# Performance work log

Hardware: AMD Instinct MI355X
Metric: run time of the kernel (lower is better)

## Reference

```python
import jax, jax.numpy as jnp
from jax import lax
import numpy as np

MAX_SEQ_LEN = 8192
B, S, D = 8, 8192, 1024
LN_EPS = 1e-5

# ---------- static lattice structure (pure Python, replicates original incl. quirks) ----------

def _gen_spine(max_len):
    s = [0, 2, 4]
    while True:
        nxt = 2 * s[-1] + 2 * s[-2] + 2 * s[-3]
        if nxt >= max_len:
            break
        s.append(nxt)
    return s

def _imm_anc(spine, pos):
    if pos in spine:
        i = spine.index(pos)
        if i >= 3:
            return [spine[i - 1], spine[i - 2], spine[i - 3]]
    return []

def _analyze(spine, pos):
    # BFS over ancestors; NOTE: levels[level+1] is OVERWRITTEN per popped node,
    # exactly as in the original torch code.
    visited = {pos}
    levels = {0: [pos]}
    queue = [(pos, 0)]
    while queue:
        cur, lvl = queue.pop(0)
        if lvl >= 9:
            break
        newl = []
        for a in _imm_anc(spine, cur):
            if a not in visited and a >= 0:
                visited.add(a)
                newl.append(a)
                queue.append((a, lvl + 1))
        if newl:
            levels[lvl + 1] = list(newl)
    max_depth = max(levels.keys())
    pc = {pos: 1}
    for lvl in sorted(levels.keys(), reverse=True):
        for node in levels[lvl]:
            if node == pos:
                continue
            if lvl == max_depth:
                pc[node] = 1
                continue
            c = 0
            for ch in levels.get(lvl + 1, []):
                if node in _imm_anc(spine, ch):
                    c += pc.get(ch, 0)
            if lvl != 0:
                pc[node] = c
    pc.pop(pos, None)
    return levels, pc

def _structures(seq_len):
    spine = _gen_spine(MAX_SEQ_LEN)
    out = []
    for pos in spine:
        if pos >= seq_len or pos < 3:
            continue
        levels, pc = _analyze(spine, pos)
        anc, cnt = [], []
        for lvl in levels:  # dict insertion order == level order, as in torch
            if lvl > 0:
                for a in levels[lvl]:
                    if a < seq_len:
                        anc.append(a)
                        cnt.append(float(pc.get(a, 1)))
        if anc:
            out.append((pos, np.array(anc, np.int32), np.array(cnt, np.float32)))
    return out

# ---------- neural pieces ----------

def _gru_last(seq, w_ih, w_hh, b_ih, b_hh):
    # seq: [B, K, D]; single-layer batch_first GRU, h0 = 0; returns last hidden [B, D]
    d = w_hh.shape[1]
    def step(h, xt):
        gi = xt @ w_ih.T + b_ih   # [B, 3D]
        gh = h @ w_hh.T + b_hh
        i_r, i_z, i_n = jnp.split(gi, 3, axis=-1)
        h_r, h_z, h_n = jnp.split(gh, 3, axis=-1)
        r = jax.nn.sigmoid(i_r + h_r)
        z = jax.nn.sigmoid(i_z + h_z)
        n = jnp.tanh(i_n + r * h_n)
        return (1.0 - z) * n + z * h, None
    h0 = jnp.zeros((seq.shape[0], d), seq.dtype)
    hT, _ = lax.scan(step, h0, jnp.swapaxes(seq, 0, 1))
    return hT

def reference(x, pw_w1, pw_b1, pw_w2, pw_b2, msg_w, msg_b, ln_g, ln_b,
              gru_w_ih, gru_w_hh, gru_b_ih, gru_b_hh, gate_w, gate_b):
    structs = _structures(x.shape[1])
    out = x
    for pos, anc, cnt in structs:
        # path weights: Linear(1,64)->ReLU->Linear(64,1)->Softplus  on counts [K,1]
        c = jnp.asarray(cnt)[:, None]
        w = jax.nn.softplus(jnp.squeeze(jax.nn.relu(c @ pw_w1.T + pw_b1) @ pw_w2.T + pw_b2))  # [K]
        h_anc = x[:, anc, :]                         # [B, K, D] gather
        h_cur = x[:, pos, :]                         # [B, D]
        pair = jnp.concatenate([h_anc, jnp.broadcast_to(h_cur[:, None, :], h_anc.shape)], axis=-1)
        m = pair @ msg_w.T + msg_b                   # [B, K, D]
        mu = m.mean(-1, keepdims=True)
        var = ((m - mu) ** 2).mean(-1, keepdims=True)
        m = (m - mu) / jnp.sqrt(var + LN_EPS) * ln_g + ln_b
        m = jax.nn.gelu(m, approximate=False)
        m = m * w[None, :, None]                     # path-weighted messages
        agg = _gru_last(m, gru_w_ih, gru_w_hh, gru_b_ih, gru_b_hh)  # [B, D]
        g = jax.nn.sigmoid(jnp.concatenate([agg, h_cur], axis=-1) @ gate_w.T + gate_b)
        out = out.at[:, pos, :].set(g * agg + (1.0 - g) * h_cur)
    return out

def setup_inputs() -> dict:
    key = jax.random.key(0)
    ks = jax.random.split(key, 8)
    def n(k, shape, s=0.02):
        return jax.random.normal(k, shape, jnp.float32) * s
    return {
        "x": jax.random.normal(ks[0], (B, S, D), jnp.float32),
        "pw_w1": n(ks[1], (64, 1), 0.5), "pw_b1": jnp.zeros((64,), jnp.float32),
        "pw_w2": n(ks[2], (1, 64), 0.5), "pw_b2": jnp.zeros((1,), jnp.float32),
        "msg_w": n(ks[3], (D, 2 * D)), "msg_b": jnp.zeros((D,), jnp.float32),
        "ln_g": jnp.ones((D,), jnp.float32), "ln_b": jnp.zeros((D,), jnp.float32),
        "gru_w_ih": n(ks[4], (3 * D, D)), "gru_w_hh": n(ks[5], (3 * D, D)),
        "gru_b_ih": jnp.zeros((3 * D,), jnp.float32), "gru_b_hh": jnp.zeros((3 * D,), jnp.float32),
        "gate_w": n(ks[6], (D, 2 * D)), "gate_b": jnp.zeros((D,), jnp.float32),
    }
```

## Files before the change

### kernel.cpp

```cpp
#include <hip/hip_runtime.h>
#include <math.h>
#include <string.h>

#define SEQ 8192
#define DIM 1024
#define NBATCH 8

typedef float vf4 __attribute__((ext_vector_type(4)));

struct SDesc {
  int n, Tmax, totalRows;
  int pos[8], A[8], rowbase[8];
  int anc[8][8];
  float cnt[8][8];
  int nu;
  int upos[16];
  int up_of_s[8];
  int s_of_rr[32], a_of_rr[32], ua_of_rr[32];
};

static SDesc build_structs() {
  SDesc H{};
  int spine[24];
  int ns = 3; spine[0] = 0; spine[1] = 2; spine[2] = 4;
  for (;;) {
    long nxt = 2L * (spine[ns-1] + spine[ns-2] + spine[ns-3]);
    if (nxt >= SEQ) break;
    spine[ns++] = (int)nxt;
  }
  int rb = 0;
  for (int i = 0; i < ns; ++i) {
    int pos = spine[i];
    if (pos < 3) continue;
    bool visited[24] = {false};
    int levels[12][8]; int lcnt[12];
    for (int l = 0; l < 12; ++l) lcnt[l] = 0;
    levels[0][0] = i; lcnt[0] = 1; visited[i] = true;
    int qidx[64], qlvl[64], qh = 0, qt = 0;
    qidx[qt] = i; qlvl[qt] = 0; qt++;
    int maxd = 0;
    while (qh < qt) {
      int cur = qidx[qh], lvl = qlvl[qh]; qh++;
      if (lvl >= 9) break;
      int newl[8], nn = 0;
      if (cur >= 3) {
        for (int d = 1; d <= 3; ++d) {
          int a = cur - d;
          if (!visited[a]) { visited[a] = true; newl[nn++] = a; qidx[qt] = a; qlvl[qt] = lvl + 1; qt++; }
        }
      }
      if (nn) {
        lcnt[lvl+1] = nn;
        for (int k = 0; k < nn; ++k) levels[lvl+1][k] = newl[k];
        if (lvl + 1 > maxd) maxd = lvl + 1;
      }
    }
    float pcv[24]; bool pcs[24];
    for (int k = 0; k < 24; ++k) { pcv[k] = 0.f; pcs[k] = false; }
    pcv[i] = 1.f; pcs[i] = true;
    for (int lvl = maxd; lvl >= 0; --lvl) {
      for (int nidx = 0; nidx < lcnt[lvl]; ++nidx) {
        int node = levels[lvl][nidx];
        if (node == i) continue;
        if (lvl == maxd) { pcv[node] = 1.f; pcs[node] = true; continue; }
        float c = 0.f;
        for (int cidx = 0; cidx < lcnt[lvl+1]; ++cidx) {
          int ch = levels[lvl+1][cidx];
          if (ch >= 3 && node >= ch - 3 && node <= ch - 1) c += pcs[ch] ? pcv[ch] : 0.f;
        }
        if (lvl != 0) { pcv[node] = c; pcs[node] = true; }
      }
    }
    int A = 0;
    int sidx = H.n;
    for (int lvl = 1; lvl <= maxd; ++lvl) {
      for (int nidx = 0; nidx < lcnt[lvl]; ++nidx) {
        int node = levels[lvl][nidx];
        H.anc[sidx][A] = spine[node];
        H.cnt[sidx][A] = pcs[node] ? pcv[node] : 1.f;
        A++;
      }
    }
    if (A == 0) continue;
    H.pos[sidx] = pos; H.A[sidx] = A; H.rowbase[sidx] = rb; rb += A;
    H.n++;
  }
  H.totalRows = rb;
  H.Tmax = 0;
  for (int s = 0; s < H.n; ++s) if (H.A[s] > H.Tmax) H.Tmax = H.A[s];
  int vals[128], nv = 0;
  for (int s = 0; s < H.n; ++s) {
    vals[nv++] = H.pos[s];
    for (int a = 0; a < H.A[s]; ++a) vals[nv++] = H.anc[s][a];
  }
  H.nu = 0;
  for (int i = 0; i < nv; ++i) {
    bool seen = false;
    for (int u = 0; u < H.nu; ++u) if (H.upos[u] == vals[i]) { seen = true; break; }
    if (!seen) H.upos[H.nu++] = vals[i];
  }
  for (int i = 0; i < H.nu; ++i)
    for (int j2 = i + 1; j2 < H.nu; ++j2)
      if (H.upos[j2] < H.upos[i]) { int t = H.upos[i]; H.upos[i] = H.upos[j2]; H.upos[j2] = t; }
  auto uidx = [&](int v) { for (int u = 0; u < H.nu; ++u) if (H.upos[u] == v) return u; return 0; };
  for (int s = 0; s < H.n; ++s) {
    H.up_of_s[s] = uidx(H.pos[s]);
    for (int a = 0; a < H.A[s]; ++a) {
      int rr = H.rowbase[s] + a;
      H.s_of_rr[rr] = s; H.a_of_rr[rr] = a; H.ua_of_rr[rr] = uidx(H.anc[s][a]);
    }
  }
  return H;
}


__device__ __forceinline__ void do_copy(const vf4* __restrict__ src, vf4* __restrict__ dst,
                                        int q, int nc, int start4, int n4) {
  for (int i = q * 256 + threadIdx.x; i < n4; i += nc * 256) {
    vf4 v = __builtin_nontemporal_load(&src[start4 + i]);
    __builtin_nontemporal_store(v, &dst[start4 + i]);
  }
}

__device__ __forceinline__ float wred(float v) {
  #pragma unroll
  for (int off = 32; off; off >>= 1) v += __shfl_xor(v, off);
  return v;
}

__device__ __forceinline__ float dot4(vf4 a, vf4 b) {
  return a.x * b.x + a.y * b.y + a.z * b.z + a.w * b.w;
}


__global__ __launch_bounds__(256, 4) void k_T(SDesc sd, const float* __restrict__ x,
    const float* __restrict__ msg_w, float* __restrict__ T,
    const float* __restrict__ w1, const float* __restrict__ b1,
    const float* __restrict__ w2, const float* __restrict__ b2, float* __restrict__ wout,
    int NC, const vf4* __restrict__ csrc, vf4* __restrict__ cdst, int cstart, int cn) {
  int p = blockIdx.x;
  const int NMAIN = 1280;
  if (p == NMAIN) {
    int t = threadIdx.x;
    int s = t >> 3, a = t & 7;
    if (t < 64 && s < sd.n && a < sd.A[s]) {
      float v = sd.cnt[s][a];
      float acc = 0.f;
      for (int i = 0; i < 64; ++i) {
        float h = v * w1[i] + b1[i];
        if (h > 0.f) acc += h * w2[i];
      }
      float o = acc + b2[0];
      float sp = (o > 0.f) ? (o + log1pf(expf(-o))) : log1pf(expf(o));
      wout[s * 8 + a] = sp;
    }
    return;
  }
  if (p > NMAIN) { do_copy(csrc, cdst, p - NMAIN - 1, NC, cstart, cn); return; }
  int q = p % 128, rt = p / 128;
  int jt = (q & 7) * 16 + (q >> 3);

  int wave = threadIdx.x >> 6, lane = threadIdx.x & 63;
  int jc0 = jt * 16 + wave * 4;
  const vf4* mw4 = (const vf4*)msg_w;
  size_t b0 = (size_t)((jc0 + 0) & 1023) * 512 + (((jc0 + 0) >> 10) << 8);
  size_t b1_ = (size_t)((jc0 + 1) & 1023) * 512 + (((jc0 + 1) >> 10) << 8);
  size_t b2_ = (size_t)((jc0 + 2) & 1023) * 512 + (((jc0 + 2) >> 10) << 8);
  size_t b3 = (size_t)((jc0 + 3) & 1023) * 512 + (((jc0 + 3) >> 10) << 8);
  vf4 w0[4], w1v[4], w2v[4], w3[4];
  #pragma unroll
  for (int c = 0; c < 4; ++c) {
    w0[c]  = mw4[b0  + c * 64 + lane];
    w1v[c] = mw4[b1_ + c * 64 + lane];
    w2v[c] = mw4[b2_ + c * 64 + lane];
    w3[c]  = mw4[b3  + c * 64 + lane];
  }
  const vf4* x4 = (const vf4*)x;
  #pragma unroll 2
  for (int r = 0; r < 8; ++r) {
    int row = rt * 8 + r; int u = row >> 3, b = row & 7;
    size_t rb4 = ((size_t)b * SEQ + sd.upos[u]) * 256;
    vf4 a0 = x4[rb4 + 0 * 64 + lane], a1 = x4[rb4 + 1 * 64 + lane];
    vf4 a2 = x4[rb4 + 2 * 64 + lane], a3 = x4[rb4 + 3 * 64 + lane];
    float s0 = dot4(w0[0],  a0) + dot4(w0[1],  a1) + dot4(w0[2],  a2) + dot4(w0[3],  a3);
    float s1 = dot4(w1v[0], a0) + dot4(w1v[1], a1) + dot4(w1v[2], a2) + dot4(w1v[3], a3);
    float s2 = dot4(w2v[0], a0) + dot4(w2v[1], a1) + dot4(w2v[2], a2) + dot4(w2v[3], a3);
    float s3 = dot4(w3[0],  a0) + dot4(w3[1],  a1) + dot4(w3[2],  a2) + dot4(w3[3],  a3);
    s0 = wred(s0); s1 = wred(s1); s2 = wred(s2); s3 = wred(s3);
    if (lane == 0) {
      float* tp = T + (size_t)row * 2048 + jc0;
      tp[0] = s0; tp[1] = s1; tp[2] = s2; tp[3] = s3;
    }
  }
}

__global__ __launch_bounds__(256) void k_ln(SDesc sd, const float* __restrict__ ln_g,
    const float* __restrict__ ln_b, const float* __restrict__ msg_b,
    const float* __restrict__ wsc, const float* __restrict__ T, float* __restrict__ mseq,
    int M, int NC, const vf4* __restrict__ csrc, vf4* __restrict__ cdst, int cstart, int cn) {
  int p = blockIdx.x;
  if (p >= M) { do_copy(csrc, cdst, p - M, NC, cstart, cn); return; }
  int rr = p >> 3, b = p & 7;
  int s = sd.s_of_rr[rr], a = sd.a_of_rr[rr];
  int ua = sd.ua_of_rr[rr], up = sd.up_of_s[s];
  float wmul = wsc[s * 8 + a];
  const vf4* Tl = (const vf4*)(T + ((size_t)ua * 8 + b) * 2048);
  const vf4* Tr = (const vf4*)(T + ((size_t)up * 8 + b) * 2048 + 1024);
  const vf4* mb = (const vf4*)msg_b;
  int t = threadIdx.x;
  vf4 vl = Tl[t], vr = Tr[t], vb = mb[t];
  vf4 v; v.x = vl.x + vr.x + vb.x; v.y = vl.y + vr.y + vb.y;
  v.z = vl.z + vr.z + vb.z; v.w = vl.w + vr.w + vb.w;
  float sum = v.x + v.y + v.z + v.w;
  float sq  = v.x * v.x + v.y * v.y + v.z * v.z + v.w * v.w;
  #pragma unroll
  for (int off = 32; off; off >>= 1) { sum += __shfl_xor(sum, off); sq += __shfl_xor(sq, off); }
  __shared__ float s1[4], s2[4];
  int wave = t >> 6, lane = t & 63;
  if (lane == 0) { s1[wave] = sum; s2[wave] = sq; }
  __syncthreads();
  sum = s1[0] + s1[1] + s1[2] + s1[3];
  sq  = s2[0] + s2[1] + s2[2] + s2[3];
  float mu  = sum * (1.f / 1024.f);
  float var = sq * (1.f / 1024.f) - mu * mu;
  float inv = rsqrtf(var + 1e-5f);
  vf4 g4 = ((const vf4*)ln_g)[t];
  vf4 b4 = ((const vf4*)ln_b)[t];
  float o[4]  = {v.x, v.y, v.z, v.w};
  float gg[4] = {g4.x, g4.y, g4.z, g4.w};
  float bb[4] = {b4.x, b4.y, b4.z, b4.w};
  #pragma unroll
  for (int i = 0; i < 4; ++i) {
    float u = (o[i] - mu) * inv * gg[i] + bb[i];
    float ge = 0.5f * u * (1.f + erff(u * 0.70710678118654752f));
    o[i] = ge * wmul;
  }
  vf4 ov; ov.x = o[0]; ov.y = o[1]; ov.z = o[2]; ov.w = o[3];
  ((vf4*)(mseq + (size_t)p * DIM))[t] = ov;
}

__global__ __launch_bounds__(256, 4) void k_gi(const float* __restrict__ mseq,
    const float* __restrict__ wih, const float* __restrict__ bih, float* __restrict__ gi,
    int NC, const vf4* __restrict__ csrc, vf4* __restrict__ cdst, int cstart, int cn) {
  int p = blockIdx.x;
  const int NMAIN = 2880;
  if (p >= NMAIN) { do_copy(csrc, cdst, p - NMAIN, NC, cstart, cn); return; }
  int q = p % 192, rt = p / 192;
  int jt = (q & 7) * 24 + (q >> 3);

  int wave = threadIdx.x >> 6, lane = threadIdx.x & 63;
  int j0 = jt * 16 + wave * 4;
  const vf4* wp4 = (const vf4*)wih;
  vf4 w0[4], w1[4], w2[4], w3[4];
  #pragma unroll
  for (int c = 0; c < 4; ++c) {
    w0[c] = wp4[(size_t)(j0 + 0) * 256 + c * 64 + lane];
    w1[c] = wp4[(size_t)(j0 + 1) * 256 + c * 64 + lane];
    w2[c] = wp4[(size_t)(j0 + 2) * 256 + c * 64 + lane];
    w3[c] = wp4[(size_t)(j0 + 3) * 256 + c * 64 + lane];
  }
  const vf4* m4 = (const vf4*)mseq;
  #pragma unroll 2
  for (int r = 0; r < 16; ++r) {
    int row = rt * 16 + r;
    size_t rb4 = (size_t)row * 256;
    vf4 a0 = m4[rb4 + 0 * 64 + lane], a1 = m4[rb4 + 1 * 64 + lane];
    vf4 a2 = m4[rb4 + 2 * 64 + lane], a3 = m4[rb4 + 3 * 64 + lane];
    float s0 = dot4(w0[0], a0) + dot4(w0[1], a1) + dot4(w0[2], a2) + dot4(w0[3], a3);
    float s1 = dot4(w1[0], a0) + dot4(w1[1], a1) + dot4(w1[2], a2) + dot4(w1[3], a3);
    float s2 = dot4(w2[0], a0) + dot4(w2[1], a1) + dot4(w2[2], a2) + dot4(w2[3], a3);
    float s3 = dot4(w3[0], a0) + dot4(w3[1], a1) + dot4(w3[2], a2) + dot4(w3[3], a3);
    s0 = wred(s0); s1 = wred(s1); s2 = wred(s2); s3 = wred(s3);
    if (lane == 0) {
      float* gp = gi + (size_t)row * 3072 + j0;
      gp[0] = s0 + bih[j0 + 0]; gp[1] = s1 + bih[j0 + 1];
      gp[2] = s2 + bih[j0 + 2]; gp[3] = s3 + bih[j0 + 3];
    }
  }
}

__global__ __launch_bounds__(256, 4) void k_step(SDesc sd, int t,
    const float* __restrict__ whh, const float* __restrict__ bhh,
    const float* __restrict__ gi, const float* __restrict__ hold, float* __restrict__ hnew,
    int NC, const vf4* __restrict__ csrc, vf4* __restrict__ cdst, int cstart, int cn) {
  int p = blockIdx.x;
  const int NMAIN = 7 * 256;
  if (p >= NMAIN) { do_copy(csrc, cdst, p - NMAIN, NC, cstart, cn); return; }
  int q = p & 255, s = p >> 8;
  int jt = (q & 7) * 32 + (q >> 3);
  int t0 = sd.Tmax - sd.A[s];
  if (t < t0) return;
  int a = t - t0;

  int wave = threadIdx.x >> 6, lane = threadIdx.x & 63;
  int j = jt * 4 + wave;
  int girow0 = (sd.rowbase[s] + a) * 8;

  if (a == 0) {
    if (lane < 8) {
      int r = lane;
      const float* gp = gi + (size_t)(girow0 + r) * 3072;
      float rg = 1.f / (1.f + expf(-(gp[j] + bhh[j])));
      float zg = 1.f / (1.f + expf(-(gp[1024 + j] + bhh[1024 + j])));
      float ng = tanhf(gp[2048 + j] + rg * bhh[2048 + j]);
      hnew[(size_t)(s * 8 + r) * DIM + j] = (1.f - zg) * ng;
    }
    return;
  }

  const vf4* wp4 = (const vf4*)whh;
  vf4 wr[4], wz[4], wn[4];
  #pragma unroll
  for (int c = 0; c < 4; ++c) {
    wr[c] = wp4[(size_t)j * 256 + c * 64 + lane];
    wz[c] = wp4[(size_t)(1024 + j) * 256 + c * 64 + lane];
    wn[c] = wp4[(size_t)(2048 + j) * 256 + c * 64 + lane];
  }
  float bj_r = bhh[j], bj_z = bhh[1024 + j], bj_n = bhh[2048 + j];
  const vf4* h4 = (const vf4*)hold;
  #pragma unroll 2
  for (int r = 0; r < 8; ++r) {
    int srow = s * 8 + r;
    size_t rb4 = (size_t)srow * 256;
    const float* gp = gi + (size_t)(girow0 + r) * 3072;
    float gir = gp[j], giz = gp[1024 + j], gin = gp[2048 + j];
    vf4 a0 = h4[rb4 + 0 * 64 + lane], a1 = h4[rb4 + 1 * 64 + lane];
    vf4 a2 = h4[rb4 + 2 * 64 + lane], a3 = h4[rb4 + 3 * 64 + lane];
    float ar = dot4(wr[0], a0) + dot4(wr[1], a1) + dot4(wr[2], a2) + dot4(wr[3], a3);
    float az = dot4(wz[0], a0) + dot4(wz[1], a1) + dot4(wz[2], a2) + dot4(wz[3], a3);
    float an = dot4(wn[0], a0) + dot4(wn[1], a1) + dot4(wn[2], a2) + dot4(wn[3], a3);
    ar = wred(ar); az = wred(az); an = wred(an);
    if (lane == 0) {
      float rg = 1.f / (1.f + expf(-(gir + ar + bj_r)));
      float zg = 1.f / (1.f + expf(-(giz + az + bj_z)));
      float ng = tanhf(gin + rg * (an + bj_n));
      float ho = hold[(size_t)srow * DIM + j];
      hnew[(size_t)srow * DIM + j] = (1.f - zg) * ng + zg * ho;
    }
  }
}

__global__ __launch_bounds__(256, 4) void k_gate(SDesc sd, const float* __restrict__ x,
    const float* __restrict__ gw, const float* __restrict__ gb,
    const float* __restrict__ hfin, float* __restrict__ out) {
  int p = blockIdx.x;
  int q = p % 128, rt = p / 128;
  int jt = (q & 7) * 16 + (q >> 3);

  int wave = threadIdx.x >> 6, lane = threadIdx.x & 63;
  int j0 = jt * 8 + wave * 2;
  const vf4* g4p = (const vf4*)gw;
  vf4 wL0[4], wR0[4], wL1[4], wR1[4];
  #pragma unroll
  for (int c = 0; c < 4; ++c) {
    wL0[c] = g4p[(size_t)(j0 + 0) * 512 + c * 64 + lane];
    wR0[c] = g4p[(size_t)(j0 + 0) * 512 + 256 + c * 64 + lane];
    wL1[c] = g4p[(size_t)(j0 + 1) * 512 + c * 64 + lane];
    wR1[c] = g4p[(size_t)(j0 + 1) * 512 + 256 + c * 64 + lane];
  }
  const vf4* h4 = (const vf4*)hfin;
  const vf4* x4 = (const vf4*)x;
  #pragma unroll 2
  for (int r = 0; r < 8; ++r) {
    int row = rt * 8 + r; int s = row >> 3, b = row & 7;
    size_t ab4 = (size_t)row * 256;
    size_t xb4 = ((size_t)b * SEQ + sd.pos[s]) * 256;
    vf4 a0 = h4[ab4 + 0 * 64 + lane], a1 = h4[ab4 + 1 * 64 + lane];
    vf4 a2 = h4[ab4 + 2 * 64 + lane], a3 = h4[ab4 + 3 * 64 + lane];
    vf4 x0 = x4[xb4 + 0 * 64 + lane], x1 = x4[xb4 + 1 * 64 + lane];
    vf4 x2 = x4[xb4 + 2 * 64 + lane], x3 = x4[xb4 + 3 * 64 + lane];
    float s0 = dot4(wL0[0], a0) + dot4(wL0[1], a1) + dot4(wL0[2], a2) + dot4(wL0[3], a3)
             + dot4(wR0[0], x0) + dot4(wR0[1], x1) + dot4(wR0[2], x2) + dot4(wR0[3], x3);
    float s1 = dot4(wL1[0], a0) + dot4(wL1[1], a1) + dot4(wL1[2], a2) + dot4(wL1[3], a3)
             + dot4(wR1[0], x0) + dot4(wR1[1], x1) + dot4(wR1[2], x2) + dot4(wR1[3], x3);
    s0 = wred(s0); s1 = wred(s1);
    if (lane == 0) {
      #pragma unroll
      for (int jj = 0; jj < 2; ++jj) {
        int j = j0 + jj;
        float sv = jj ? s1 : s0;
        float g = 1.f / (1.f + expf(-(sv + gb[j])));
        float agg = hfin[(size_t)row * DIM + j];
        float hc  = x[((size_t)b * SEQ + sd.pos[s]) * DIM + j];
        out[((size_t)b * SEQ + sd.pos[s]) * DIM + j] = g * agg + (1.f - g) * hc;
      }
    }
  }
}


extern "C" void kernel_launch(void* const* d_in, const int* in_sizes, int n_in,
                              void* d_out, int out_size, void* d_ws, size_t ws_size,
                              hipStream_t stream) {
  const float* x      = (const float*)d_in[0];
  const float* pw_w1  = (const float*)d_in[1];
  const float* pw_b1  = (const float*)d_in[2];
  const float* pw_w2  = (const float*)d_in[3];
  const float* pw_b2  = (const float*)d_in[4];
  const float* msg_w  = (const float*)d_in[5];
  const float* msg_b  = (const float*)d_in[6];
  const float* ln_g   = (const float*)d_in[7];
  const float* ln_b   = (const float*)d_in[8];
  const float* w_ih   = (const float*)d_in[9];
  const float* w_hh   = (const float*)d_in[10];
  const float* b_ih   = (const float*)d_in[11];
  const float* b_hh   = (const float*)d_in[12];
  const float* gate_w = (const float*)d_in[13];
  const float* gate_b = (const float*)d_in[14];
  float* out = (float*)d_out;
  float* ws  = (float*)d_ws;

  SDesc sd = build_structs();
  const int M = sd.totalRows * 8;

  float* wout = ws;
  float* T    = wout + 64;
  float* mseq = T + (size_t)sd.nu * 8 * 2048;
  float* gi   = mseq + (size_t)240 * DIM;
  float* h0   = gi + (size_t)240 * 3072;
  float* h1   = h0 + (size_t)sd.n * 8 * DIM;

  const vf4* x4 = (const vf4*)x;
  vf4* out4 = (vf4*)out;
  const int TOTAL4 = (NBATCH * SEQ * DIM) / 4;

  const int c_T  = 2200000;
  const int c_ln = 2400000;
  const int c_gi = 1800000;
  const int c_s0 = 2600000;
  const int c_s  = 1900000;

  int off = 0;
  k_T<<<1280 + 1 + 1024, 256, 0, stream>>>(sd, x, msg_w, T,
                                           pw_w1, pw_b1, pw_w2, pw_b2, wout,
                                           1024, x4, out4, off, c_T);
  off += c_T;

  k_ln<<<M + 1280, 256, 0, stream>>>(sd, ln_g, ln_b, msg_b, wout, T, mseq,
                                     M, 1280, x4, out4, off, c_ln);
  off += c_ln;

  k_gi<<<2880 + 1024, 256, 0, stream>>>(mseq, w_ih, b_ih, gi, 1024, x4, out4, off, c_gi);
  off += c_gi;

  for (int t = 0; t < sd.Tmax; ++t) {
    const float* hr = (t & 1) ? h1 : h0;
    float*       hw = (t & 1) ? h0 : h1;
    int cnt = (t == 0) ? c_s0 : (t == sd.Tmax - 1) ? (TOTAL4 - off) : c_s;
    k_step<<<7 * 256 + 1280, 256, 0, stream>>>(sd, t, w_hh, b_hh, gi, hr, hw,
                                               1280, x4, out4, off, cnt);
    off += cnt;
  }
  const float* hfin = (sd.Tmax & 1) ? h1 : h0;

  k_gate<<<128 * 7, 256, 0, stream>>>(sd, x, gate_w, gate_b, hfin, out);

  (void)in_sizes; (void)n_in; (void)out_size; (void)ws_size;
}
```

Baseline: 266.1 us.

## Fold background copy into all blocks, hoist GRU step 0, shrink grids

Drops the dedicated copy-only blocks. Every block of each phase kernel now runs its compute work and then takes a grid-strided share of the x→out copy. The first GRU step (zero hidden state) moves into the input-projection kernel, so the step loop runs from t=1 to 4 with Tmax hardcoded. The step and gate kernels now loop over all structures inside one block instead of spreading them over blocks, which cuts the grid size and reloads fewer weights. The price is less parallelism in the recurrent steps and hardcoded structure constants (Tmax, 240 rows, 56 rows). The k_gi launch also covers only 1920 of the 240×3072 outputs per row tile, with 24 rows per block, and its correctness depends on that arithmetic.

```diff
diff --git a/kernel.cpp b/kernel.cpp
--- a/kernel.cpp
+++ b/kernel.cpp
@@ -1,6 +1,5 @@
 #include <hip/hip_runtime.h>
 #include <math.h>
-#include <string.h>
 
 #define SEQ 8192
 #define DIM 1024
@@ -114,14 +113,6 @@
 }
 
 
-__device__ __forceinline__ void do_copy(const vf4* __restrict__ src, vf4* __restrict__ dst,
-                                        int q, int nc, int start4, int n4) {
-  for (int i = q * 256 + threadIdx.x; i < n4; i += nc * 256) {
-    vf4 v = __builtin_nontemporal_load(&src[start4 + i]);
-    __builtin_nontemporal_store(v, &dst[start4 + i]);
-  }
-}
-
 __device__ __forceinline__ float wred(float v) {
   #pragma unroll
   for (int off = 32; off; off >>= 1) v += __shfl_xor(v, off);
@@ -132,12 +123,21 @@
   return a.x * b.x + a.y * b.y + a.z * b.z + a.w * b.w;
 }
 
+__device__ __forceinline__ void phase_copy(const vf4* __restrict__ src,
+                                           vf4* __restrict__ dst, int start, int cnt) {
+  int stride = gridDim.x * 256;
+  for (int i = blockIdx.x * 256 + threadIdx.x; i < cnt; i += stride) {
+    vf4 v = __builtin_nontemporal_load(&src[start + i]);
+    __builtin_nontemporal_store(v, &dst[start + i]);
+  }
+}
+
 
 __global__ __launch_bounds__(256, 4) void k_T(SDesc sd, const float* __restrict__ x,
     const float* __restrict__ msg_w, float* __restrict__ T,
     const float* __restrict__ w1, const float* __restrict__ b1,
     const float* __restrict__ w2, const float* __restrict__ b2, float* __restrict__ wout,
-    int NC, const vf4* __restrict__ csrc, vf4* __restrict__ cdst, int cstart, int cn) {
+    const vf4* __restrict__ csrc, vf4* __restrict__ cdst, int cstart, int cn) {
   int p = blockIdx.x;
   const int NMAIN = 1280;
   if (p == NMAIN) {
@@ -151,163 +151,167 @@
         if (h > 0.f) acc += h * w2[i];
       }
       float o = acc + b2[0];
-      float sp = (o > 0.f) ? (o + log1pf(expf(-o))) : log1pf(expf(o));
-      wout[s * 8 + a] = sp;
-    }
-    return;
-  }
-  if (p > NMAIN) { do_copy(csrc, cdst, p - NMAIN - 1, NC, cstart, cn); return; }
-  int q = p % 128, rt = p / 128;
-  int jt = (q & 7) * 16 + (q >> 3);
-
-  int wave = threadIdx.x >> 6, lane = threadIdx.x & 63;
-  int jc0 = jt * 16 + wave * 4;
-  const vf4* mw4 = (const vf4*)msg_w;
-  size_t b0 = (size_t)((jc0 + 0) & 1023) * 512 + (((jc0 + 0) >> 10) << 8);
-  size_t b1_ = (size_t)((jc0 + 1) & 1023) * 512 + (((jc0 + 1) >> 10) << 8);
-  size_t b2_ = (size_t)((jc0 + 2) & 1023) * 512 + (((jc0 + 2) >> 10) << 8);
-  size_t b3 = (size_t)((jc0 + 3) & 1023) * 512 + (((jc0 + 3) >> 10) << 8);
-  vf4 w0[4], w1v[4], w2v[4], w3[4];
-  #pragma unroll
-  for (int c = 0; c < 4; ++c) {
-    w0[c]  = mw4[b0  + c * 64 + lane];
-    w1v[c] = mw4[b1_ + c * 64 + lane];
-    w2v[c] = mw4[b2_ + c * 64 + lane];
-    w3[c]  = mw4[b3  + c * 64 + lane];
-  }
-  const vf4* x4 = (const vf4*)x;
-  #pragma unroll 2
-  for (int r = 0; r < 8; ++r) {
-    int row = rt * 8 + r; int u = row >> 3, b = row & 7;
-    size_t rb4 = ((size_t)b * SEQ + sd.upos[u]) * 256;
-    vf4 a0 = x4[rb4 + 0 * 64 + lane], a1 = x4[rb4 + 1 * 64 + lane];
-    vf4 a2 = x4[rb4 + 2 * 64 + lane], a3 = x4[rb4 + 3 * 64 + lane];
-    float s0 = dot4(w0[0],  a0) + dot4(w0[1],  a1) + dot4(w0[2],  a2) + dot4(w0[3],  a3);
-    float s1 = dot4(w1v[0], a0) + dot4(w1v[1], a1) + dot4(w1v[2], a2) + dot4(w1v[3], a3);
-    float s2 = dot4(w2v[0], a0) + dot4(w2v[1], a1) + dot4(w2v[2], a2) + dot4(w2v[3], a3);
-    float s3 = dot4(w3[0],  a0) + dot4(w3[1],  a1) + dot4(w3[2],  a2) + dot4(w3[3],  a3);
-    s0 = wred(s0); s1 = wred(s1); s2 = wred(s2); s3 = wred(s3);
-    if (lane == 0) {
-      float* tp = T + (size_t)row * 2048 + jc0;
-      tp[0] = s0; tp[1] = s1; tp[2] = s2; tp[3] = s3;
-    }
-  }
+      wout[s * 8 + a] = (o > 0.f) ? (o + log1pf(expf(-o))) : log1pf(expf(o));
+    }
+  } else {
+    int q = p % 128, rt = p / 128;
+    int jt = (q & 7) * 16 + (q >> 3);
+    int wave = threadIdx.x >> 6, lane = threadIdx.x & 63;
+    int jc0 = jt * 16 + wave * 4;
+    const vf4* mw4 = (const vf4*)msg_w;
+    size_t wb0 = (size_t)((jc0 + 0) & 1023) * 512 + ((size_t)((jc0 + 0) >> 10) << 8);
+    size_t wb1 = (size_t)((jc0 + 1) & 1023) * 512 + ((size_t)((jc0 + 1) >> 10) << 8);
+    size_t wb2 = (size_t)((jc0 + 2) & 1023) * 512 + ((size_t)((jc0 + 2) >> 10) << 8);
+    size_t wb3 = (size_t)((jc0 + 3) & 1023) * 512 + ((size_t)((jc0 + 3) >> 10) << 8);
+    vf4 tw0[4], tw1[4], tw2[4], tw3[4];
+    #pragma unroll
+    for (int c = 0; c < 4; ++c) {
+      tw0[c] = mw4[wb0 + c * 64 + lane];
+      tw1[c] = mw4[wb1 + c * 64 + lane];
+      tw2[c] = mw4[wb2 + c * 64 + lane];
+      tw3[c] = mw4[wb3 + c * 64 + lane];
+    }
+    const vf4* x4 = (const vf4*)x;
+    #pragma unroll 2
+    for (int r = 0; r < 8; ++r) {
+      int row = rt * 8 + r; int uq = row >> 3, bb = row & 7;
+      size_t rb4 = ((size_t)bb * SEQ + sd.upos[uq]) * 256;
+      vf4 a0 = x4[rb4 + 0 * 64 + lane], a1 = x4[rb4 + 1 * 64 + lane];
+      vf4 a2 = x4[rb4 + 2 * 64 + lane], a3 = x4[rb4 + 3 * 64 + lane];
+      float s0 = dot4(tw0[0], a0) + dot4(tw0[1], a1) + dot4(tw0[2], a2) + dot4(tw0[3], a3);
+      float s1 = dot4(tw1[0], a0) + dot4(tw1[1], a1) + dot4(tw1[2], a2) + dot4(tw1[3], a3);
+      float s2 = dot4(tw2[0], a0) + dot4(tw2[1], a1) + dot4(tw2[2], a2) + dot4(tw2[3], a3);
+      float s3 = dot4(tw3[0], a0) + dot4(tw3[1], a1) + dot4(tw3[2], a2) + dot4(tw3[3], a3);
+      s0 = wred(s0); s1 = wred(s1); s2 = wred(s2); s3 = wred(s3);
+      if (lane == 0) {
+        float* tp = T + (size_t)row * 2048 + jc0;
+        tp[0] = s0; tp[1] = s1; tp[2] = s2; tp[3] = s3;
+      }
+    }
+  }
+  phase_copy(csrc, cdst, cstart, cn);
 }
 
 __global__ __launch_bounds__(256) void k_ln(SDesc sd, const float* __restrict__ ln_g,
     const float* __restrict__ ln_b, const float* __restrict__ msg_b,
     const float* __restrict__ wsc, const float* __restrict__ T, float* __restrict__ mseq,
-    int M, int NC, const vf4* __restrict__ csrc, vf4* __restrict__ cdst, int cstart, int cn) {
+    const vf4* __restrict__ csrc, vf4* __restrict__ cdst, int cstart, int cn) {
   int p = blockIdx.x;
-  if (p >= M) { do_copy(csrc, cdst, p - M, NC, cstart, cn); return; }
-  int rr = p >> 3, b = p & 7;
-  int s = sd.s_of_rr[rr], a = sd.a_of_rr[rr];
-  int ua = sd.ua_of_rr[rr], up = sd.up_of_s[s];
-  float wmul = wsc[s * 8 + a];
-  const vf4* Tl = (const vf4*)(T + ((size_t)ua * 8 + b) * 2048);
-  const vf4* Tr = (const vf4*)(T + ((size_t)up * 8 + b) * 2048 + 1024);
-  const vf4* mb = (const vf4*)msg_b;
-  int t = threadIdx.x;
-  vf4 vl = Tl[t], vr = Tr[t], vb = mb[t];
-  vf4 v; v.x = vl.x + vr.x + vb.x; v.y = vl.y + vr.y + vb.y;
-  v.z = vl.z + vr.z + vb.z; v.w = vl.w + vr.w + vb.w;
-  float sum = v.x + v.y + v.z + v.w;
-  float sq  = v.x * v.x + v.y * v.y + v.z * v.z + v.w * v.w;
-  #pragma unroll
-  for (int off = 32; off; off >>= 1) { sum += __shfl_xor(sum, off); sq += __shfl_xor(sq, off); }
-  __shared__ float s1[4], s2[4];
-  int wave = t >> 6, lane = t & 63;
-  if (lane == 0) { s1[wave] = sum; s2[wave] = sq; }
-  __syncthreads();
-  sum = s1[0] + s1[1] + s1[2] + s1[3];
-  sq  = s2[0] + s2[1] + s2[2] + s2[3];
-  float mu  = sum * (1.f / 1024.f);
-  float var = sq * (1.f / 1024.f) - mu * mu;
-  float inv = rsqrtf(var + 1e-5f);
-  vf4 g4 = ((const vf4*)ln_g)[t];
-  vf4 b4 = ((const vf4*)ln_b)[t];
-  float o[4]  = {v.x, v.y, v.z, v.w};
-  float gg[4] = {g4.x, g4.y, g4.z, g4.w};
-  float bb[4] = {b4.x, b4.y, b4.z, b4.w};
-  #pragma unroll
-  for (int i = 0; i < 4; ++i) {
-    float u = (o[i] - mu) * inv * gg[i] + bb[i];
-    float ge = 0.5f * u * (1.f + erff(u * 0.70710678118654752f));
-    o[i] = ge * wmul;
-  }
-  vf4 ov; ov.x = o[0]; ov.y = o[1]; ov.z = o[2]; ov.w = o[3];
-  ((vf4*)(mseq + (size_t)p * DIM))[t] = ov;
-}
-
-__global__ __launch_bounds__(256, 4) void k_gi(const float* __restrict__ mseq,
-    const float* __restrict__ wih, const float* __restrict__ bih, float* __restrict__ gi,
-    int NC, const vf4* __restrict__ csrc, vf4* __restrict__ cdst, int cstart, int cn) {
+  if (p < 240) {
+    int rr = p >> 3, bb = p & 7;
+    int s = sd.s_of_rr[rr], aa = sd.a_of_rr[rr];
+    int ua = sd.ua_of_rr[rr], up = sd.up_of_s[s];
+    float wmul = wsc[s * 8 + aa];
+    const vf4* Tl = (const vf4*)(T + ((size_t)ua * 8 + bb) * 2048);
+    const vf4* Tr = (const vf4*)(T + ((size_t)up * 8 + bb) * 2048 + 1024);
+    const vf4* mb = (const vf4*)msg_b;
+    int t = threadIdx.x;
+    vf4 vl = Tl[t], vr = Tr[t], vb = mb[t];
+    vf4 v; v.x = vl.x + vr.x + vb.x; v.y = vl.y + vr.y + vb.y;
+    v.z = vl.z + vr.z + vb.z; v.w = vl.w + vr.w + vb.w;
+    float sum = v.x + v.y + v.z + v.w;
+    float sq  = v.x * v.x + v.y * v.y + v.z * v.z + v.w * v.w;
+    #pragma unroll
+    for (int off = 32; off; off >>= 1) { sum += __shfl_xor(sum, off); sq += __shfl_xor(sq, off); }
+    __shared__ float s1[4], s2[4];
+    int wave = t >> 6, lane = t & 63;
+    if (lane == 0) { s1[wave] = sum; s2[wave] = sq; }
+    __syncthreads();
+    sum = s1[0] + s1[1] + s1[2] + s1[3];
+    sq  = s2[0] + s2[1] + s2[2] + s2[3];
+    float mu  = sum * (1.f / 1024.f);
+    float var = sq * (1.f / 1024.f) - mu * mu;
+    float inv = rsqrtf(var + 1e-5f);
+    vf4 g4 = ((const vf4*)ln_g)[t];
+    vf4 b4 = ((const vf4*)ln_b)[t];
+    float o[4]  = {v.x, v.y, v.z, v.w};
+    float gg[4] = {g4.x, g4.y, g4.z, g4.w};
+    float bb2[4] = {b4.x, b4.y, b4.z, b4.w};
+    #pragma unroll
+    for (int i = 0; i < 4; ++i) {
+      float u = (o[i] - mu) * inv * gg[i] + bb2[i];
+      float ge = 0.5f * u * (1.f + erff(u * 0.70710678118654752f));
+      o[i] = ge * wmul;
+    }
+    vf4 ov; ov.x = o[0]; ov.y = o[1]; ov.z = o[2]; ov.w = o[3];
+    ((vf4*)(mseq + (size_t)p * DIM))[t] = ov;
+  }
+  phase_copy(csrc, cdst, cstart, cn);
+}
+
+__global__ __launch_bounds__(256, 4) void k_gi(SDesc sd, const float* __restrict__ mseq,
+    const float* __restrict__ wih, const float* __restrict__ bih,
+    const float* __restrict__ bhh, float* __restrict__ gi, float* __restrict__ h1,
+    const vf4* __restrict__ csrc, vf4* __restrict__ cdst, int cstart, int cn) {
   int p = blockIdx.x;
-  const int NMAIN = 2880;
-  if (p >= NMAIN) { do_copy(csrc, cdst, p - NMAIN, NC, cstart, cn); return; }
-  int q = p % 192, rt = p / 192;
-  int jt = (q & 7) * 24 + (q >> 3);
-
-  int wave = threadIdx.x >> 6, lane = threadIdx.x & 63;
-  int j0 = jt * 16 + wave * 4;
-  const vf4* wp4 = (const vf4*)wih;
-  vf4 w0[4], w1[4], w2[4], w3[4];
-  #pragma unroll
-  for (int c = 0; c < 4; ++c) {
-    w0[c] = wp4[(size_t)(j0 + 0) * 256 + c * 64 + lane];
-    w1[c] = wp4[(size_t)(j0 + 1) * 256 + c * 64 + lane];
-    w2[c] = wp4[(size_t)(j0 + 2) * 256 + c * 64 + lane];
-    w3[c] = wp4[(size_t)(j0 + 3) * 256 + c * 64 + lane];
-  }
-  const vf4* m4 = (const vf4*)mseq;
-  #pragma unroll 2
-  for (int r = 0; r < 16; ++r) {
-    int row = rt * 16 + r;
-    size_t rb4 = (size_t)row * 256;
-    vf4 a0 = m4[rb4 + 0 * 64 + lane], a1 = m4[rb4 + 1 * 64 + lane];
-    vf4 a2 = m4[rb4 + 2 * 64 + lane], a3 = m4[rb4 + 3 * 64 + lane];
-    float s0 = dot4(w0[0], a0) + dot4(w0[1], a1) + dot4(w0[2], a2) + dot4(w0[3], a3);
-    float s1 = dot4(w1[0], a0) + dot4(w1[1], a1) + dot4(w1[2], a2) + dot4(w1[3], a3);
-    float s2 = dot4(w2[0], a0) + dot4(w2[1], a1) + dot4(w2[2], a2) + dot4(w2[3], a3);
-    float s3 = dot4(w3[0], a0) + dot4(w3[1], a1) + dot4(w3[2], a2) + dot4(w3[3], a3);
-    s0 = wred(s0); s1 = wred(s1); s2 = wred(s2); s3 = wred(s3);
-    if (lane == 0) {
-      float* gp = gi + (size_t)row * 3072 + j0;
-      gp[0] = s0 + bih[j0 + 0]; gp[1] = s1 + bih[j0 + 1];
-      gp[2] = s2 + bih[j0 + 2]; gp[3] = s3 + bih[j0 + 3];
-    }
-  }
+  {
+    int q = p % 192, rt = p / 192;
+    int jt = (q & 7) * 24 + (q >> 3);
+    int wave = threadIdx.x >> 6, lane = threadIdx.x & 63;
+    int j0 = jt * 16 + wave * 4;
+    const vf4* wp4 = (const vf4*)wih;
+    vf4 w0[4], w1[4], w2[4], w3[4];
+    #pragma unroll
+    for (int c = 0; c < 4; ++c) {
+      w0[c] = wp4[(size_t)(j0 + 0) * 256 + c * 64 + lane];
+      w1[c] = wp4[(size_t)(j0 + 1) * 256 + c * 64 + lane];
+      w2[c] = wp4[(size_t)(j0 + 2) * 256 + c * 64 + lane];
+      w3[c] = wp4[(size_t)(j0 + 3) * 256 + c * 64 + lane];
+    }
+    const vf4* m4 = (const vf4*)mseq;
+    for (int r = 0; r < 24; ++r) {
+      int row = rt * 24 + r;
+      size_t rb4 = (size_t)row * 256;
+      vf4 a0 = m4[rb4 + 0 * 64 + lane], a1 = m4[rb4 + 1 * 64 + lane];
+      vf4 a2 = m4[rb4 + 2 * 64 + lane], a3 = m4[rb4 + 3 * 64 + lane];
+      float s0 = dot4(w0[0], a0) + dot4(w0[1], a1) + dot4(w0[2], a2) + dot4(w0[3], a3);
+      float s1 = dot4(w1[0], a0) + dot4(w1[1], a1) + dot4(w1[2], a2) + dot4(w1[3], a3);
+      float s2 = dot4(w2[0], a0) + dot4(w2[1], a1) + dot4(w2[2], a2) + dot4(w2[3], a3);
+      float s3 = dot4(w3[0], a0) + dot4(w3[1], a1) + dot4(w3[2], a2) + dot4(w3[3], a3);
+      s0 = wred(s0); s1 = wred(s1); s2 = wred(s2); s3 = wred(s3);
+      if (lane == 0) {
+        float sv[4] = {s0, s1, s2, s3};
+        float* gp = gi + (size_t)row * 3072;
+        int rr = row >> 3;
+        int s = sd.s_of_rr[rr];
+        bool st0 = (sd.a_of_rr[rr] == 0 && sd.A[s] == sd.Tmax);
+        #pragma unroll
+        for (int jj = 0; jj < 4; ++jj) {
+          int jg = j0 + jj;
+          float val = sv[jj] + bih[jg];
+          gp[jg] = val;
+        }
+        if (st0) {
+        }
+      }
+    }
+  }
+  {
+    int tid = blockIdx.x * 256 + threadIdx.x;
+    int total = 240 * DIM;
+    for (int i = tid; i < total; i += gridDim.x * 256) {
+      int row = i >> 10, j = i & 1023;
+      int rr = row >> 3;
+      int s = sd.s_of_rr[rr];
+      if (sd.a_of_rr[rr] == 0 && sd.A[s] == sd.Tmax) {
+        const float* gp = gi + (size_t)row * 3072;
+        float rg = 1.f / (1.f + expf(-(gp[j] + bhh[j])));
+        float zg = 1.f / (1.f + expf(-(gp[1024 + j] + bhh[1024 + j])));
+        float ng = tanhf(gp[2048 + j] + rg * bhh[2048 + j]);
+        h1[(size_t)(s * 8 + (row & 7)) * DIM + j] = (1.f - zg) * ng;
+      }
+    }
+  }
+  phase_copy(csrc, cdst, cstart, cn);
 }
 
 __global__ __launch_bounds__(256, 4) void k_step(SDesc sd, int t,
     const float* __restrict__ whh, const float* __restrict__ bhh,
     const float* __restrict__ gi, const float* __restrict__ hold, float* __restrict__ hnew,
-    int NC, const vf4* __restrict__ csrc, vf4* __restrict__ cdst, int cstart, int cn) {
+    const vf4* __restrict__ csrc, vf4* __restrict__ cdst, int cstart, int cn) {
   int p = blockIdx.x;
-  const int NMAIN = 7 * 256;
-  if (p >= NMAIN) { do_copy(csrc, cdst, p - NMAIN, NC, cstart, cn); return; }
-  int q = p & 255, s = p >> 8;
-  int jt = (q & 7) * 32 + (q >> 3);
-  int t0 = sd.Tmax - sd.A[s];
-  if (t < t0) return;
-  int a = t - t0;
-
   int wave = threadIdx.x >> 6, lane = threadIdx.x & 63;
-  int j = jt * 4 + wave;
-  int girow0 = (sd.rowbase[s] + a) * 8;
-
-  if (a == 0) {
-    if (lane < 8) {
-      int r = lane;
-      const float* gp = gi + (size_t)(girow0 + r) * 3072;
-      float rg = 1.f / (1.f + expf(-(gp[j] + bhh[j])));
-      float zg = 1.f / (1.f + expf(-(gp[1024 + j] + bhh[1024 + j])));
-      float ng = tanhf(gp[2048 + j] + rg * bhh[2048 + j]);
-      hnew[(size_t)(s * 8 + r) * DIM + j] = (1.f - zg) * ng;
-    }
-    return;
-  }
-
+  int j = p * 4 + wave;
   const vf4* wp4 = (const vf4*)whh;
   vf4 wr[4], wz[4], wn[4];
   #pragma unroll
@@ -318,37 +322,53 @@
   }
   float bj_r = bhh[j], bj_z = bhh[1024 + j], bj_n = bhh[2048 + j];
   const vf4* h4 = (const vf4*)hold;
-  #pragma unroll 2
-  for (int r = 0; r < 8; ++r) {
-    int srow = s * 8 + r;
-    size_t rb4 = (size_t)srow * 256;
-    const float* gp = gi + (size_t)(girow0 + r) * 3072;
-    float gir = gp[j], giz = gp[1024 + j], gin = gp[2048 + j];
-    vf4 a0 = h4[rb4 + 0 * 64 + lane], a1 = h4[rb4 + 1 * 64 + lane];
-    vf4 a2 = h4[rb4 + 2 * 64 + lane], a3 = h4[rb4 + 3 * 64 + lane];
-    float ar = dot4(wr[0], a0) + dot4(wr[1], a1) + dot4(wr[2], a2) + dot4(wr[3], a3);
-    float az = dot4(wz[0], a0) + dot4(wz[1], a1) + dot4(wz[2], a2) + dot4(wz[3], a3);
-    float an = dot4(wn[0], a0) + dot4(wn[1], a1) + dot4(wn[2], a2) + dot4(wn[3], a3);
-    ar = wred(ar); az = wred(az); an = wred(an);
-    if (lane == 0) {
-      float rg = 1.f / (1.f + expf(-(gir + ar + bj_r)));
-      float zg = 1.f / (1.f + expf(-(giz + az + bj_z)));
-      float ng = tanhf(gin + rg * (an + bj_n));
-      float ho = hold[(size_t)srow * DIM + j];
-      hnew[(size_t)srow * DIM + j] = (1.f - zg) * ng + zg * ho;
-    }
-  }
+  for (int s = 0; s < 7; ++s) {
+    if (s >= sd.n) break;
+    int t0 = sd.Tmax - sd.A[s];
+    if (t < t0) continue;
+    int a = t - t0;
+    int girow0 = (sd.rowbase[s] + a) * 8;
+    if (a == 0) {
+      if (lane < 8) {
+        int r = lane;
+        const float* gp = gi + (size_t)(girow0 + r) * 3072;
+        float rg = 1.f / (1.f + expf(-(gp[j] + bj_r)));
+        float zg = 1.f / (1.f + expf(-(gp[1024 + j] + bj_z)));
+        float ng = tanhf(gp[2048 + j] + rg * bj_n);
+        hnew[(size_t)(s * 8 + r) * DIM + j] = (1.f - zg) * ng;
+      }
+      continue;
+    }
+    #pragma unroll 2
+    for (int r = 0; r < 8; ++r) {
+      int srow = s * 8 + r;
+      size_t rb4 = (size_t)srow * 256;
+      const float* gp = gi + (size_t)(girow0 + r) * 3072;
+      float gir = gp[j], giz = gp[1024 + j], gin = gp[2048 + j];
+      vf4 a0 = h4[rb4 + 0 * 64 + lane], a1 = h4[rb4 + 1 * 64 + lane];
+      vf4 a2 = h4[rb4 + 2 * 64 + lane], a3 = h4[rb4 + 3 * 64 + lane];
+      float ar = dot4(wr[0], a0) + dot4(wr[1], a1) + dot4(wr[2], a2) + dot4(wr[3], a3);
+      float az = dot4(wz[0], a0) + dot4(wz[1], a1) + dot4(wz[2], a2) + dot4(wz[3], a3);
+      float an = dot4(wn[0], a0) + dot4(wn[1], a1) + dot4(wn[2], a2) + dot4(wn[3], a3);
+      ar = wred(ar); az = wred(az); an = wred(an);
+      if (lane == 0) {
+        float rg = 1.f / (1.f + expf(-(gir + ar + bj_r)));
+        float zg = 1.f / (1.f + expf(-(giz + az + bj_z)));
+        float ng = tanhf(gin + rg * (an + bj_n));
+        float ho = hold[(size_t)srow * DIM + j];
+        hnew[(size_t)srow * DIM + j] = (1.f - zg) * ng + zg * ho;
+      }
+    }
+  }
+  phase_copy(csrc, cdst, cstart, cn);
 }
 
 __global__ __launch_bounds__(256, 4) void k_gate(SDesc sd, const float* __restrict__ x,
     const float* __restrict__ gw, const float* __restrict__ gb,
     const float* __restrict__ hfin, float* __restrict__ out) {
   int p = blockIdx.x;
-  int q = p % 128, rt = p / 128;
-  int jt = (q & 7) * 16 + (q >> 3);
-
   int wave = threadIdx.x >> 6, lane = threadIdx.x & 63;
-  int j0 = jt * 8 + wave * 2;
+  int j0 = p * 8 + wave * 2;
   const vf4* g4p = (const vf4*)gw;
   vf4 wL0[4], wR0[4], wL1[4], wR1[4];
   #pragma unroll
@@ -360,11 +380,10 @@
   }
   const vf4* h4 = (const vf4*)hfin;
   const vf4* x4 = (const vf4*)x;
-  #pragma unroll 2
-  for (int r = 0; r < 8; ++r) {
-    int row = rt * 8 + r; int s = row >> 3, b = row & 7;
+  for (int row = 0; row < 56; ++row) {
+    int s = row >> 3, bb = row & 7;
     size_t ab4 = (size_t)row * 256;
-    size_t xb4 = ((size_t)b * SEQ + sd.pos[s]) * 256;
+    size_t xb4 = ((size_t)bb * SEQ + sd.pos[s]) * 256;
     vf4 a0 = h4[ab4 + 0 * 64 + lane], a1 = h4[ab4 + 1 * 64 + lane];
     vf4 a2 = h4[ab4 + 2 * 64 + lane], a3 = h4[ab4 + 3 * 64 + lane];
     vf4 x0 = x4[xb4 + 0 * 64 + lane], x1 = x4[xb4 + 1 * 64 + lane];
@@ -381,8 +400,8 @@
         float sv = jj ? s1 : s0;
         float g = 1.f / (1.f + expf(-(sv + gb[j])));
         float agg = hfin[(size_t)row * DIM + j];
-        float hc  = x[((size_t)b * SEQ + sd.pos[s]) * DIM + j];
-        out[((size_t)b * SEQ + sd.pos[s]) * DIM + j] = g * agg + (1.f - g) * hc;
+        float hc  = x[((size_t)bb * SEQ + sd.pos[s]) * DIM + j];
+        out[((size_t)bb * SEQ + sd.pos[s]) * DIM + j] = g * agg + (1.f - g) * hc;
       }
     }
   }
@@ -411,7 +430,6 @@
   float* ws  = (float*)d_ws;
 
   SDesc sd = build_structs();
-  const int M = sd.totalRows * 8;
 
   float* wout = ws;
   float* T    = wout + 64;
@@ -423,37 +441,32 @@
   const vf4* x4 = (const vf4*)x;
   vf4* out4 = (vf4*)out;
   const int TOTAL4 = (NBATCH * SEQ * DIM) / 4;
-
-  const int c_T  = 2200000;
-  const int c_ln = 2400000;
-  const int c_gi = 1800000;
-  const int c_s0 = 2600000;
-  const int c_s  = 1900000;
+  const int c_T = 3200000, c_ln = 3600000, c_gi = 3300000, c_s = 1660000;
 
   int off = 0;
-  k_T<<<1280 + 1 + 1024, 256, 0, stream>>>(sd, x, msg_w, T,
-                                           pw_w1, pw_b1, pw_w2, pw_b2, wout,
-                                           1024, x4, out4, off, c_T);
+  k_T<<<1281, 256, 0, stream>>>(sd, x, msg_w, T, pw_w1, pw_b1, pw_w2, pw_b2, wout,
+                                x4, out4, off, c_T);
   off += c_T;
 
-  k_ln<<<M + 1280, 256, 0, stream>>>(sd, ln_g, ln_b, msg_b, wout, T, mseq,
-                                     M, 1280, x4, out4, off, c_ln);
+  k_ln<<<1024, 256, 0, stream>>>(sd, ln_g, ln_b, msg_b, wout, T, mseq,
+                                 x4, out4, off, c_ln);
   off += c_ln;
 
-  k_gi<<<2880 + 1024, 256, 0, stream>>>(mseq, w_ih, b_ih, gi, 1024, x4, out4, off, c_gi);
+  k_gi<<<1920, 256, 0, stream>>>(sd, mseq, w_ih, b_ih, b_hh, gi, h1,
+                                 x4, out4, off, c_gi);
   off += c_gi;
 
-  for (int t = 0; t < sd.Tmax; ++t) {
+  for (int t = 1; t <= 4; ++t) {
     const float* hr = (t & 1) ? h1 : h0;
     float*       hw = (t & 1) ? h0 : h1;
-    int cnt = (t == 0) ? c_s0 : (t == sd.Tmax - 1) ? (TOTAL4 - off) : c_s;
-    k_step<<<7 * 256 + 1280, 256, 0, stream>>>(sd, t, w_hh, b_hh, gi, hr, hw,
-                                               1280, x4, out4, off, cnt);
+    int cnt = (t == 4) ? (TOTAL4 - off) : c_s;
+    k_step<<<256, 256, 0, stream>>>(sd, t, w_hh, b_hh, gi, hr, hw,
+                                    x4, out4, off, cnt);
     off += cnt;
   }
-  const float* hfin = (sd.Tmax & 1) ? h1 : h0;
-
-  k_gate<<<128 * 7, 256, 0, stream>>>(sd, x, gate_w, gate_b, hfin, out);
+  const float* hfin = h1;
+
+  k_gate<<<128, 256, 0, stream>>>(sd, x, gate_w, gate_b, hfin, out);
 
   (void)in_sizes; (void)n_in; (void)out_size; (void)ws_size;
 }
```

After: 484.5 us. +82.1%, slower.
